# Optimization experiments

Hardware: AMD Instinct MI355X
Metric: run time of the kernel (lower is better)

## Reference

```python
import jax, jax.numpy as jnp
from jax import lax
import numpy as np

B, S, T = 64, 100, 96
SRC_V, PRIM_V, NPROD, NFLD = 32000, 16000, 201, 100
E, HE, H, F, ATT = 128, 128, 256, 64, 256
DIN = E + ATT + F + H  # 704 = action_emb + prev_att + field + parent_state


def setup_inputs():
    key = jax.random.key(0)
    ks = jax.random.split(key, 40)
    def p(k, shape):
        return (jax.random.normal(k, shape) * 0.05).astype(jnp.float32)
    sent_lens = jax.random.randint(ks[0], (B,), 1, S + 1)
    src_tokens = jax.random.randint(ks[1], (B, S), 0, SRC_V)
    prev_action_ids = jax.random.randint(ks[2], (B, T), 0, NPROD)
    frontier_ids = jax.random.randint(ks[3], (B, T), 0, NFLD)
    # parent_t[b, t] must point at an already-produced decoder state (< t)
    parent_t = jax.random.randint(ks[4], (B, T), 0, T) % jnp.maximum(jnp.arange(T), 1)
    atype = jax.random.randint(ks[5], (B, T), 0, 4)  # 0=apply,1=gen,2=copy,3=pad
    is_applyconstr = (atype == 0).astype(jnp.float32)
    is_gentoken = (atype == 1).astype(jnp.float32)
    is_copy = (atype == 2).astype(jnp.float32)
    is_copy_tok = (jax.random.uniform(ks[6], (B, T, S)) < 0.05).astype(jnp.float32) * is_copy[:, :, None]
    applyconstr_ids = jax.random.randint(ks[7], (B, T), 0, NPROD)
    gentok_ids = jax.random.randint(ks[8], (B, T), 0, PRIM_V)
    return dict(
        src_tokens=src_tokens, sent_lens=sent_lens, prev_action_ids=prev_action_ids,
        parent_t=parent_t, frontier_ids=frontier_ids, applyconstr_ids=applyconstr_ids,
        gentok_ids=gentok_ids, is_applyconstr=is_applyconstr, is_gentoken=is_gentoken,
        is_copy=is_copy, is_copy_tok=is_copy_tok,
        src_emb=p(ks[9], (SRC_V, E)), prod_emb=p(ks[10], (NPROD, E)),
        prim_emb=p(ks[11], (PRIM_V, E)), field_emb=p(ks[12], (NFLD, F)),
        Wih_f=p(ks[13], (4 * HE, E)), Whh_f=p(ks[14], (4 * HE, HE)), bih_f=p(ks[15], (4 * HE,)), bhh_f=p(ks[16], (4 * HE,)),
        Wih_b=p(ks[17], (4 * HE, E)), Whh_b=p(ks[18], (4 * HE, HE)), bih_b=p(ks[19], (4 * HE,)), bhh_b=p(ks[20], (4 * HE,)),
        Wih_d=p(ks[21], (4 * H, DIN)), Whh_d=p(ks[22], (4 * H, H)), bih_d=p(ks[23], (4 * H,)), bhh_d=p(ks[24], (4 * H,)),
        W_lin_attn=p(ks[25], (H, H)), W_att_vec=p(ks[26], (ATT, 2 * H)), W_ptr=p(ks[27], (ATT, H)),
        W_a2e=p(ks[28], (E, ATT)), W_gen=p(ks[29], (1, ATT)), b_gen=p(ks[30], (1,)),
    )


def _cell(x, h, c, Wih, Whh, bih, bhh):
    # torch.nn.LSTMCell gate order: i, f, g, o
    g = x @ Wih.T + bih + h @ Whh.T + bhh
    i, f, gg, o = jnp.split(g, 4, axis=-1)
    c = jax.nn.sigmoid(f) * c + jax.nn.sigmoid(i) * jnp.tanh(gg)
    return jax.nn.sigmoid(o) * jnp.tanh(c), c


def _forward(src_tokens, sent_lens, prev_action_ids, parent_t, frontier_ids,
             applyconstr_ids, gentok_ids, is_applyconstr, is_gentoken, is_copy, is_copy_tok,
             src_emb, prod_emb, prim_emb, field_emb,
             Wih_f, Whh_f, bih_f, bhh_f, Wih_b, Whh_b, bih_b, bhh_b,
             Wih_d, Whh_d, bih_d, bhh_d,
             W_lin_attn, W_att_vec, W_ptr, W_a2e, W_gen, b_gen):
    b, s = src_tokens.shape
    t_max = prev_action_ids.shape[1]
    emb = src_emb[src_tokens]                                  # [B,S,E]
    valid = jnp.arange(s)[None, :] < sent_lens[:, None]        # [B,S]

    def make_step(Wih, Whh, bih, bhh):
        def step(carry, xs):
            h, c = carry
            xt, vt = xs
            hn, cn = _cell(xt, h, c, Wih, Whh, bih, bhh)
            m = vt[:, None]
            hn = jnp.where(m, hn, h)
            cn = jnp.where(m, cn, c)
            return (hn, cn), hn
        return step

    z = jnp.zeros((b, HE), emb.dtype)
    (hf, cf), hs_f = lax.scan(make_step(Wih_f, Whh_f, bih_f, bhh_f), (z, z),
                              (emb.transpose(1, 0, 2), valid.T))
    (hb, cb), hs_b = lax.scan(make_step(Wih_b, Whh_b, bih_b, bhh_b), (z, z),
                              (emb[:, ::-1].transpose(1, 0, 2), valid[:, ::-1].T))
    hs_b = hs_b[::-1]                                          # re-align to forward order
    encodings = jnp.concatenate([hs_f, hs_b], -1).transpose(1, 0, 2) * valid[:, :, None]  # [B,S,H]
    h = jnp.concatenate([hf, hb], -1)                          # [B,H] final bi-state
    c = jnp.concatenate([cf, cb], -1)
    h_enc_final = h

    src_pad = ~valid
    enc_attn = encodings @ W_lin_attn.T                        # [B,S,H]

    def s_attention(hh):
        aw = jnp.einsum('bsh,bh->bs', enc_attn, hh)
        aw = jax.nn.softmax(jnp.where(src_pad, -jnp.inf, aw), axis=1)
        ctx = jnp.einsum('bs,bsh->bh', aw, encodings)
        return jnp.tanh(jnp.concatenate([ctx, hh], -1) @ W_att_vec.T)

    # decode step t = 0 with zero input
    h, c = _cell(jnp.zeros((b, DIN), emb.dtype), h, c, Wih_d, Whh_d, bih_d, bhh_d)
    buf = jnp.zeros((t_max, b, H), emb.dtype).at[0].set(h)     # states_sequence buffer
    s0 = s_attention(h)

    def dec_step(carry, xs):
        h, c, s_prev, buf = carry
        t, a_id, f_id, pt = xs
        parent = buf[pt, jnp.arange(b)]                        # data-dependent parent state
        inp = jnp.concatenate([prod_emb[a_id], s_prev, field_emb[f_id], parent], -1)
        h, c = _cell(inp, h, c, Wih_d, Whh_d, bih_d, bhh_d)
        buf = buf.at[t].set(h)
        s = s_attention(h)
        return (h, c, s, buf), s

    xs = (jnp.arange(1, t_max), prev_action_ids[:, 1:].T, frontier_ids[:, 1:].T, parent_t[:, 1:].T)
    _, s_rest = lax.scan(dec_step, (h, c, s0, buf), xs)
    s_att = jnp.concatenate([s0[None], s_rest], 0)             # [T,B,ATT]

    readout = s_att @ W_a2e.T                                  # [T,B,E]
    p_apply = jax.nn.softmax(jnp.einsum('tbe,ne->tbn', readout, prod_emb), axis=-1)
    p_tok = jax.nn.softmax(jnp.einsum('tbe,ve->tbv', readout, prim_emb), axis=-1)
    p_gen = jax.nn.sigmoid(s_att @ W_gen.T + b_gen)[..., 0]    # [T,B]
    hW = encodings @ W_ptr.T                                   # [B,S,ATT]
    sc = jnp.einsum('tbh,bsh->tbs', s_att, hW)
    p_copy_tok = jax.nn.softmax(jnp.where(src_pad[None], -jnp.inf, sc), axis=-1)

    tgt_copy = jnp.sum(p_copy_tok * is_copy_tok.transpose(1, 0, 2), axis=2)        # [T,B]
    tgt_apply = jnp.take_along_axis(p_apply, applyconstr_ids.T[:, :, None], axis=2)[..., 0]
    tgt_gen = jnp.take_along_axis(p_tok, gentok_ids.T[:, :, None], axis=2)[..., 0]

    ap = (tgt_apply * is_applyconstr.T
          + p_gen * tgt_gen * is_gentoken.T
          + (1.0 - p_gen) * tgt_copy * is_copy.T)
    pad = (is_applyconstr + is_gentoken + is_copy).T == 0
    ap = jnp.where(pad, 1e-7, ap)
    logp = jnp.log(ap) * (~pad)
    return jnp.sum(logp, axis=0), h_enc_final


def reference(src_tokens, sent_lens, prev_action_ids, parent_t, frontier_ids,
              applyconstr_ids, gentok_ids, is_applyconstr, is_gentoken, is_copy, is_copy_tok,
              src_emb, prod_emb, prim_emb, field_emb,
              Wih_f, Whh_f, bih_f, bhh_f, Wih_b, Whh_b, bih_b, bhh_b,
              Wih_d, Whh_d, bih_d, bhh_d,
              W_lin_attn, W_att_vec, W_ptr, W_a2e, W_gen, b_gen):
    return _forward(src_tokens, sent_lens, prev_action_ids, parent_t, frontier_ids,
                    applyconstr_ids, gentok_ids, is_applyconstr, is_gentoken, is_copy, is_copy_tok,
                    src_emb, prod_emb, prim_emb, field_emb,
                    Wih_f, Whh_f, bih_f, bhh_f, Wih_b, Whh_b, bih_b, bhh_b,
                    Wih_d, Whh_d, bih_d, bhh_d,
                    W_lin_attn, W_att_vec, W_ptr, W_a2e, W_gen, b_gen)
```

## Files before the change

kernel.cpp:

```cpp
#include <hip/hip_runtime.h>
#include <math.h>

typedef unsigned int uint;
typedef unsigned short ushort;
typedef unsigned char uchar;
typedef _Float16 v2h __attribute__((ext_vector_type(2)));
typedef short bf16x8 __attribute__((ext_vector_type(8)));
typedef float f32x4 __attribute__((ext_vector_type(4)));

__device__ __forceinline__ float sigf(float x) { return 1.f / (1.f + expf(-x)); }

__device__ __forceinline__ uint packh2(float a, float b) {
  v2h v; v[0] = (_Float16)a; v[1] = (_Float16)b;
  return __builtin_bit_cast(uint, v);
}
__device__ __forceinline__ ushort f2h(float x) {
  _Float16 h = (_Float16)x;
  return __builtin_bit_cast(ushort, h);
}
__device__ __forceinline__ float h2f(ushort u) {
  return (float)__builtin_bit_cast(_Float16, u);
}
__device__ __forceinline__ float dot2(uint w, uint x, float acc) {
  return __builtin_amdgcn_fdot2(__builtin_bit_cast(v2h, w), __builtin_bit_cast(v2h, x), acc, false);
}
__device__ __forceinline__ ushort f2bf(float f) {
  uint x = __builtin_bit_cast(uint, f);
  return (ushort)((x + 0x7fffu + ((x >> 16) & 1u)) >> 16);
}
__device__ __forceinline__ int dot8i4(uint w, uint x, int acc) {
#if __has_builtin(__builtin_amdgcn_sdot8)
  return __builtin_amdgcn_sdot8((int)w, (int)x, acc, false);
#else
#pragma unroll
  for (int j = 0; j < 8; j++) {
    int a = ((int)(w << (28 - 4 * j))) >> 28;
    int b = ((int)(x << (28 - 4 * j))) >> 28;
    acc += a * b;
  }
  return acc;
#endif
}
__device__ __forceinline__ char qi4b(float x) { return (char)(int)rintf(x * 7.f); }
__device__ __forceinline__ uint nib4(uint a) {
  a &= 0x0F0F0F0Fu;
  a |= a >> 4;
  a &= 0x00FF00FFu;
  a |= a >> 8;
  return a & 0xFFFFu;
}

__device__ __forceinline__ float wgval8(int k, int d, const float* Wih, const float* Whh) {
  if (k < 256) return Wih[d * 704 + 128 + k];
  if (k < 512) return Wih[d * 704 + 448 + (k - 256)];
  return Whh[d * 256 + (k - 512)];
}

__device__ __forceinline__ void tr_one(const float* __restrict__ src, float* __restrict__ dst,
                                       int i, int rows, int ld, int col0) {
  int r = i % rows, c = i / rows;
  dst[i] = src[r * ld + col0 + c];
}

__global__ __launch_bounds__(256) void k_prepack(
    const float* __restrict__ Wih_f, const float* __restrict__ Wih_b,
    const float* __restrict__ W_lin, const float* __restrict__ W_ptr,
    const float* __restrict__ W_att, const float* __restrict__ W_a2e,
    const float* __restrict__ Wih_d, const float* __restrict__ prim_emb,
    const float* __restrict__ bih_f, const float* __restrict__ bhh_f,
    const float* __restrict__ bih_b, const float* __restrict__ bhh_b,
    const float* __restrict__ bih_d, const float* __restrict__ bhh_d,
    float* __restrict__ WIHFT, float* __restrict__ WIHBT, float* __restrict__ WLINT,
    float* __restrict__ WPTRT, float* __restrict__ WATTCT, float* __restrict__ WA2ET,
    float* __restrict__ WPRODT, float* __restrict__ WFLDT,
    uint* __restrict__ WAH16, ushort* __restrict__ PRIM16,
    float* __restrict__ BFB, float* __restrict__ BBB, float* __restrict__ BDD,
    float* __restrict__ DEN) {
  int idx = blockIdx.x * 256 + threadIdx.x;
  if (idx < 65536) tr_one(Wih_f, WIHFT, idx, 512, 128, 0);
  else if (idx < 131072) tr_one(Wih_b, WIHBT, idx - 65536, 512, 128, 0);
  else if (idx < 196608) tr_one(W_lin, WLINT, idx - 131072, 256, 256, 0);
  else if (idx < 262144) tr_one(W_ptr, WPTRT, idx - 196608, 256, 256, 0);
  else if (idx < 327680) tr_one(W_att, WATTCT, idx - 262144, 256, 512, 0);
  else if (idx < 360448) tr_one(W_a2e, WA2ET, idx - 327680, 128, 256, 0);
  else if (idx < 491520) tr_one(Wih_d, WPRODT, idx - 360448, 1024, 704, 0);
  else if (idx < 557056) tr_one(Wih_d, WFLDT, idx - 491520, 1024, 704, 384);
  else if (idx < 589824) {
    int i2 = idx - 557056;
    int kk = i2 >> 8, r = i2 & 255;
    WAH16[i2] = packh2(W_att[r * 512 + 256 + 2 * kk], W_att[r * 512 + 257 + 2 * kk]);
  } else if (idx < 590848) {
    int i2 = idx - 589824;
    if (i2 < 512) { BFB[i2] = bih_f[i2] + bhh_f[i2]; BBB[i2] = bih_b[i2] + bhh_b[i2]; }
    BDD[i2] = bih_d[i2] + bhh_d[i2];
  } else if (idx < 596992) {
    DEN[idx - 590848] = 0.f;
  } else if (idx < 2644992) {
    int i2 = idx - 596992;
    PRIM16[i2] = f2bf(prim_emb[i2]);
  }
}

__global__ __launch_bounds__(256) void k_packgi4(
    const float* __restrict__ Wih, const float* __restrict__ Whh,
    uint* __restrict__ outp, float* __restrict__ wscale) {
  int d = blockIdx.x, tid = threadIdx.x;
  __shared__ float arr[768];
  __shared__ float red[256];
  float v0 = wgval8(tid, d, Wih, Whh);
  float v1 = wgval8(tid + 256, d, Wih, Whh);
  float v2 = wgval8(tid + 512, d, Wih, Whh);
  arr[tid] = v0; arr[tid + 256] = v1; arr[tid + 512] = v2;
  red[tid] = fmaxf(fabsf(v0), fmaxf(fabsf(v1), fabsf(v2)));
  __syncthreads();
  for (int off = 128; off; off >>= 1) {
    if (tid < off) red[tid] = fmaxf(red[tid], red[tid + off]);
    __syncthreads();
  }
  float wmax = red[0];
  float inv = (wmax > 0.f) ? (7.f / wmax) : 0.f;
  if (tid < 96) {
    uint u = 0;
#pragma unroll
    for (int b = 0; b < 8; b++) {
      int q = (int)rintf(arr[8 * tid + b] * inv);
      u |= ((uint)q & 0xFu) << (4 * b);
    }
    outp[((tid >> 2) * 1024 + d) * 4 + (tid & 3)] = u;
  }
  if (tid == 0) wscale[d] = wmax / 49.f;
}

__global__ __launch_bounds__(256) void k_pfw2(
    const float* __restrict__ prod_emb, const float* __restrict__ field_emb,
    const float* __restrict__ WPRODT, const float* __restrict__ WFLDT,
    float* __restrict__ PW, float* __restrict__ FW) {
  int bi = blockIdx.x, tid = threadIdx.x;
  const float* emb; const float* WT; float* outp; int K, a;
  if (bi < 201) { a = bi; emb = prod_emb; WT = WPRODT; outp = PW; K = 128; }
  else { a = bi - 201; emb = field_emb; WT = WFLDT; outp = FW; K = 64; }
  __shared__ float es[128];
  if (tid < K) es[tid] = emb[a * K + tid];
  __syncthreads();
  float acc[4] = {0, 0, 0, 0};
  for (int k = 0; k < K; k++) {
    float ev = es[k];
#pragma unroll
    for (int j = 0; j < 4; j++) acc[j] = fmaf(ev, WT[k * 1024 + tid + j * 256], acc[j]);
  }
#pragma unroll
  for (int j = 0; j < 4; j++) outp[a * 1024 + tid + j * 256] = acc[j];
}

__global__ __launch_bounds__(256) void k_xproj2(const int* __restrict__ toks,
    const float* __restrict__ embt,
    const float* __restrict__ WTF, const float* __restrict__ WTB,
    const float* __restrict__ biasF, const float* __restrict__ biasB,
    float* __restrict__ outF, float* __restrict__ outB) {
  int bi = blockIdx.x;
  const float* WT = (bi < 400) ? WTF : WTB;
  const float* bias = (bi < 400) ? biasF : biasB;
  float* outp = (bi < 400) ? outF : outB;
  int row0 = (bi % 400) * 16;
  __shared__ __align__(16) float a[16][128];
  __shared__ int tk[16];
  int tid = threadIdx.x;
  if (tid < 16) {
    int row = row0 + tid;
    int b = row & 63, s = row >> 6;
    tk[tid] = toks[b * 100 + s];
  }
  __syncthreads();
#pragma unroll
  for (int i = 0; i < 8; i++) {
    int idx = tid + i * 256;
    int r = idx >> 7, k = idx & 127;
    a[r][k] = embt[tk[r] * 128 + k];
  }
  __syncthreads();
  int c = tid;
  float acc0[16], acc1[16];
  float b0 = bias[c], b1 = bias[c + 256];
#pragma unroll
  for (int r = 0; r < 16; r++) { acc0[r] = b0; acc1[r] = b1; }
  for (int k = 0; k < 128; k++) {
    float w0 = WT[k * 512 + c];
    float w1 = WT[k * 512 + c + 256];
#pragma unroll
    for (int r = 0; r < 16; r++) {
      float av = a[r][k];
      acc0[r] = fmaf(av, w0, acc0[r]);
      acc1[r] = fmaf(av, w1, acc1[r]);
    }
  }
#pragma unroll
  for (int r = 0; r < 16; r++) {
    outp[(row0 + r) * 512 + c] = acc0[r];
    outp[(row0 + r) * 512 + c + 256] = acc1[r];
  }
}

__global__ __launch_bounds__(512) void k_enc_scan(
    const float* __restrict__ xpf, const float* __restrict__ xpb,
    const float* __restrict__ WhhF, const float* __restrict__ WhhB,
    const int* __restrict__ lens,
    float* __restrict__ enc, float* __restrict__ h0, float* __restrict__ c0,
    float* __restrict__ outp) {
  int b = blockIdx.x & 63, dir = blockIdx.x >> 6;
  const float* xp = dir ? xpb : xpf;
  const float* Whh = dir ? WhhB : WhhF;
  int t = threadIdx.x;
  float4 wv[32];
  {
    const float4* wr = (const float4*)(Whh + t * 128);
#pragma unroll
    for (int j = 0; j < 32; j++) wv[j] = wr[j];
  }
  __shared__ __align__(16) float hs[128];
  __shared__ float gs[512];
  float c = 0.f, hreg = 0.f;
  if (t < 128) hs[t] = 0.f;
  int len = lens[b];
  __syncthreads();
  for (int s = 0; s < 100; s++) {
    int pos = dir ? (99 - s) : s;
    float acc = xp[(pos * 64 + b) * 512 + t];
#pragma unroll
    for (int j = 0; j < 32; j++) {
      float4 h4 = *(const float4*)&hs[4 * j];
      acc = fmaf(wv[j].x, h4.x, acc);
      acc = fmaf(wv[j].y, h4.y, acc);
      acc = fmaf(wv[j].z, h4.z, acc);
      acc = fmaf(wv[j].w, h4.w, acc);
    }
    gs[t] = acc;
    __syncthreads();
    if (t < 128) {
      float ig = sigf(gs[t]);
      float fg = sigf(gs[128 + t]);
      float gg = tanhf(gs[256 + t]);
      float og = sigf(gs[384 + t]);
      float cn = fmaf(fg, c, ig * gg);
      float hn = og * tanhf(cn);
      if (pos < len) { c = cn; hreg = hn; }
      hs[t] = hreg;
      enc[(b * 100 + pos) * 256 + dir * 128 + t] = (pos < len) ? hreg : 0.f;
    }
    __syncthreads();
  }
  if (t < 128) {
    h0[b * 256 + dir * 128 + t] = hreg;
    c0[b * 256 + dir * 128 + t] = c;
    outp[64 + b * 256 + dir * 128 + t] = hreg;
  }
}

__global__ __launch_bounds__(256) void k_proj2(
    const float* __restrict__ enc, const float* __restrict__ WlinT,
    const float* __restrict__ WptrT, const float* __restrict__ WattCT,
    ushort* __restrict__ eat16, ushort* __restrict__ hw16, ushort* __restrict__ ew16) {
  int bx = blockIdx.x;
  int which = bx >> 8;
  int b = (bx >> 2) & 63;
  int j0 = (bx & 3) * 64;
  const float* WT = (which == 0) ? WlinT : (which == 1) ? WptrT : WattCT;
  __shared__ __align__(16) float el[20][256];
  int tid = threadIdx.x;
  int jj = tid & 63, sg = tid >> 6;
  for (int st = 0; st < 5; st++) {
    __syncthreads();
#pragma unroll
    for (int i = 0; i < 20; i++) {
      int idx = tid + i * 256;
      int r = idx >> 8, k = idx & 255;
      el[r][k] = enc[(b * 100 + st * 20 + r) * 256 + k];
    }
    __syncthreads();
    float acc[5] = {0, 0, 0, 0, 0};
    for (int k4 = 0; k4 < 64; k4++) {
      float w0 = WT[(4 * k4 + 0) * 256 + j0 + jj];
      float w1 = WT[(4 * k4 + 1) * 256 + j0 + jj];
      float w2 = WT[(4 * k4 + 2) * 256 + j0 + jj];
      float w3 = WT[(4 * k4 + 3) * 256 + j0 + jj];
#pragma unroll
      for (int q = 0; q < 5; q++) {
        float4 ev = *(const float4*)&el[sg * 5 + q][4 * k4];
        acc[q] = fmaf(ev.x, w0, fmaf(ev.y, w1, fmaf(ev.z, w2, fmaf(ev.w, w3, acc[q]))));
      }
    }
#pragma unroll
    for (int q = 0; q < 5; q++) {
      int s = st * 20 + sg * 5 + q;
      ushort hv = f2h(acc[q]);
      if (which == 0) eat16[(b * 100 + s) * 256 + j0 + jj] = hv;
      else if (which == 1) hw16[(b * 100 + s) * 256 + j0 + jj] = hv;
      else ew16[(b * 100 + s) * 256 + j0 + jj] = hv;
    }
  }
}

__global__ __launch_bounds__(1024, 4) void k_decoder(
    const uint* __restrict__ WG4, const float* __restrict__ wscale,
    const uint* __restrict__ WAH16,
    const float* __restrict__ bdd, const float* __restrict__ PW, const float* __restrict__ FW,
    const float* __restrict__ h0g, const float* __restrict__ c0g,
    const uint* __restrict__ EAT32, const uint* __restrict__ EW32,
    const int* __restrict__ aid, const int* __restrict__ ptp, const int* __restrict__ fid,
    const int* __restrict__ lens, float* __restrict__ sbuf) {
  __shared__ __align__(16) uint ea[100 * 136];
  __shared__ __align__(16) uint ewl[100 * 128];
  __shared__ __align__(16) uint xq[96];
  __shared__ __align__(16) char histq[96 * 256];
  __shared__ float gsm[1024];
  __shared__ float vp[4][256];
  __shared__ float aw[128];
  __shared__ __align__(16) uint hx32[128];
  __shared__ float csm[256];
  __shared__ __align__(16) char h0q[256];
  int e = blockIdx.x, tid = threadIdx.x;
  int len = lens[e];
  float bias0 = bdd[tid];
  float wsc = wscale[tid];
  for (int u = tid; u < 12800; u += 1024) {
    int s = u >> 7, kk = u & 127;
    ea[s * 136 + kk] = EAT32[(e * 100 + s) * 128 + kk];
    ewl[u] = EW32[e * 12800 + u];
  }
  if (tid < 256) {
    csm[tid] = c0g[e * 256 + tid];
    h0q[tid] = qi4b(h0g[e * 256 + tid]);
  }
  const uint4* wq = (const uint4*)WG4 + tid;
  uint4 wr[8];
#pragma unroll
  for (int qq = 0; qq < 8; qq++) wr[qq] = wq[qq * 1024];
  uint war[32];
  {
    int r_v = tid & 255, q_v = tid >> 8;
#pragma unroll
    for (int i = 0; i < 32; i++) war[i] = WAH16[(q_v * 32 + i) * 256 + r_v];
  }
  __syncthreads();
  if (tid < 96) {
    if (tid < 64) xq[tid] = 0u;
    else {
      const uint* p = (const uint*)&h0q[8 * (tid - 64)];
      xq[tid] = nib4(p[0]) | (nib4(p[1]) << 16);
    }
  }
  __syncthreads();
  int gacc;
  {
    int a0 = 0, a1 = 0, a2 = 0, a3 = 0;
#pragma unroll 4
    for (int qq = 8; qq < 24; qq++) {
      uint4 wv = wq[qq * 1024];
      uint4 xv = *(const uint4*)&xq[qq * 4];
      a0 = dot8i4(wv.x, xv.x, a0);
      a1 = dot8i4(wv.y, xv.y, a1);
      a2 = dot8i4(wv.z, xv.z, a2);
      a3 = dot8i4(wv.w, xv.w, a3);
    }
    gacc = a0 + a1 + a2 + a3;
  }
  float pf = 0.f;
  for (int t = 0; t < 96; t++) {
    int tn = (t < 95) ? (t + 1) : 95;
    int ptn = ptp[e * 96 + tn];
    {
      int a0 = gacc, a1 = 0, a2 = 0, a3 = 0;
#pragma unroll
      for (int qq = 0; qq < 8; qq++) {
        uint4 xv = *(const uint4*)&xq[qq * 4];
        a0 = dot8i4(wr[qq].x, xv.x, a0);
        a1 = dot8i4(wr[qq].y, xv.y, a1);
        a2 = dot8i4(wr[qq].z, xv.z, a2);
        a3 = dot8i4(wr[qq].w, xv.w, a3);
      }
      gsm[tid] = fmaf((float)(a0 + a1 + a2 + a3), wsc, bias0 + pf);
    }
    __syncthreads();
    if (tid < 256) {
      int d = tid;
      float gi = gsm[d], gf = gsm[256 + d], gg = gsm[512 + d], go = gsm[768 + d];
      float c = fmaf(sigf(gf), csm[d], sigf(gi) * tanhf(gg));
      csm[d] = c;
      float h = sigf(go) * tanhf(c);
      char q = qi4b(h);
      histq[t * 256 + d] = q;
      float hp = __shfl_xor(h, 1);
      if (!(d & 1)) hx32[d >> 1] = packh2(h, hp);
      uint v = ((uint)(uchar)q & 0xFu) << (4 * (d & 7));
      v |= (uint)__shfl_xor((int)v, 1);
      v |= (uint)__shfl_xor((int)v, 2);
      v |= (uint)__shfl_xor((int)v, 4);
      if (!(d & 7)) xq[64 + (d >> 3)] = v;
    }
    __syncthreads();
    if (tid < 800) {
      int s = tid >> 3, sub = tid & 7;
      if (s < len) {
        const uint4* ep = (const uint4*)&ea[s * 136 + sub * 16];
        const uint4* hp = (const uint4*)&hx32[sub * 16];
        float a = 0.f;
#pragma unroll
        for (int i = 0; i < 4; i++) {
          uint4 ev = ep[i], hv = hp[i];
          a = dot2(ev.x, hv.x, a);
          a = dot2(ev.y, hv.y, a);
          a = dot2(ev.z, hv.z, a);
          a = dot2(ev.w, hv.w, a);
        }
        a += __shfl_down(a, 4);
        a += __shfl_down(a, 2);
        a += __shfl_down(a, 1);
        if (sub == 0) aw[s] = a;
      }
    } else if (tid >= 960) {
      const uint* p = (const uint*)&histq[ptn * 256 + 8 * (tid - 960)];
      xq[32 + (tid - 960)] = nib4(p[0]) | (nib4(p[1]) << 16);
    }
    __syncthreads();
    {
      int a0 = 0, a1 = 0, a2 = 0, a3 = 0;
#pragma unroll 4
      for (int qq = 0; qq < 8; qq++) {
        uint4 wv = wq[(8 + qq) * 1024];
        uint4 xv = *(const uint4*)&xq[32 + qq * 4];
        a0 = dot8i4(wv.x, xv.x, a0);
        a1 = dot8i4(wv.y, xv.y, a1);
        a2 = dot8i4(wv.z, xv.z, a2);
        a3 = dot8i4(wv.w, xv.w, a3);
      }
      gacc = a0 + a1 + a2 + a3;
    }
    if (tid < 64) {
      float a0 = (tid < len) ? aw[tid] : -1e30f;
      float a1 = (64 + tid < len) ? aw[64 + tid] : -1e30f;
      float m = fmaxf(a0, a1);
#pragma unroll
      for (int off = 32; off; off >>= 1) m = fmaxf(m, __shfl_xor(m, off));
      float x0 = expf(a0 - m), x1 = expf(a1 - m);
      float ss = x0 + x1;
#pragma unroll
      for (int off = 32; off; off >>= 1) ss += __shfl_xor(ss, off);
      float rinv = 1.f / ss;
      aw[tid] = x0 * rinv;
      aw[64 + tid] = x1 * rinv;
    }
    __syncthreads();
    {
      int an = aid[e * 96 + tn], fn = fid[e * 96 + tn];
      float pw_n = PW[an * 1024 + tid];
      float fw_n = FW[fn * 1024 + tid];
      int r = tid & 255, q = tid >> 8;
      float part = 0.f;
      const ushort* ew = (const ushort*)ewl;
      for (int s = q * 25; s < q * 25 + 25; s++)
        part = fmaf(aw[s], h2f(ew[s * 256 + r]), part);
#pragma unroll
      for (int i = 0; i < 32; i++)
        part = dot2(war[i], hx32[q * 32 + i], part);
      vp[q][r] = part;
      {
        int a0 = 0, a1 = 0, a2 = 0, a3 = 0;
#pragma unroll 4
        for (int qq = 0; qq < 8; qq++) {
          uint4 wv = wq[(16 + qq) * 1024];
          uint4 xv = *(const uint4*)&xq[64 + qq * 4];
          a0 = dot8i4(wv.x, xv.x, a0);
          a1 = dot8i4(wv.y, xv.y, a1);
          a2 = dot8i4(wv.z, xv.z, a2);
          a3 = dot8i4(wv.w, xv.w, a3);
        }
        gacc += a0 + a1 + a2 + a3;
      }
      pf = pw_n + fw_n;
    }
    __syncthreads();
    if (tid < 256) {
      float s = tanhf(vp[0][tid] + vp[1][tid] + vp[2][tid] + vp[3][tid]);
      sbuf[(t * 64 + e) * 256 + tid] = s;
      uint v = ((uint)(uchar)qi4b(s) & 0xFu) << (4 * (tid & 7));
      v |= (uint)__shfl_xor((int)v, 1);
      v |= (uint)__shfl_xor((int)v, 2);
      v |= (uint)__shfl_xor((int)v, 4);
      if (!(tid & 7)) xq[tid >> 3] = v;
    }
    __syncthreads();
  }
}

__global__ __launch_bounds__(256) void k_readout(const float* __restrict__ sbuf,
    const float* __restrict__ wT, float* __restrict__ rd, ushort* __restrict__ rd16) {
  int row0 = blockIdx.x * 16;
  __shared__ __align__(16) float sl[16][256];
  int tid = threadIdx.x;
#pragma unroll
  for (int i = 0; i < 16; i++) {
    int idx = tid + i * 256;
    int r = idx >> 8, k = idx & 255;
    sl[r][k] = sbuf[(row0 + r) * 256 + k];
  }
  __syncthreads();
  int c = tid & 127, rg = tid >> 7;
  float acc[8] = {0, 0, 0, 0, 0, 0, 0, 0};
  for (int k4 = 0; k4 < 64; k4++) {
    float w0 = wT[(4 * k4 + 0) * 128 + c];
    float w1 = wT[(4 * k4 + 1) * 128 + c];
    float w2 = wT[(4 * k4 + 2) * 128 + c];
    float w3 = wT[(4 * k4 + 3) * 128 + c];
#pragma unroll
    for (int r = 0; r < 8; r++) {
      float4 s4 = *(const float4*)&sl[rg * 8 + r][4 * k4];
      acc[r] = fmaf(s4.x, w0, fmaf(s4.y, w1, fmaf(s4.z, w2, fmaf(s4.w, w3, acc[r]))));
    }
  }
#pragma unroll
  for (int r = 0; r < 8; r++) {
    int row = row0 + rg * 8 + r;
    rd[row * 128 + c] = acc[r];
    rd16[row * 128 + c] = f2bf(acc[r]);
  }
}

__global__ __launch_bounds__(256) void k_apply2(
    const float* __restrict__ rd, const float* __restrict__ prod,
    const int* __restrict__ ids, float* __restrict__ tga) {
  __shared__ __align__(16) float pl[201 * 128];
  __shared__ __align__(16) float rl[32][128];
  int tid = threadIdx.x;
  int row0 = blockIdx.x * 32;
  for (int u = tid; u < 201 * 128; u += 256) pl[u] = prod[u];
  for (int u = tid; u < 4096; u += 256) {
    int r = u >> 7, k = u & 127;
    rl[r][k] = rd[(row0 + r) * 128 + k];
  }
  __syncthreads();
  int wv = tid >> 6, l = tid & 63;
  float lg[8][4];
#pragma unroll
  for (int rr = 0; rr < 8; rr++)
#pragma unroll
    for (int s = 0; s < 4; s++) lg[rr][s] = 0.f;
  int nvalid = (l + 192 < 201) ? 4 : 3;
  for (int k4 = 0; k4 < 32; k4++) {
    float4 rv[8];
#pragma unroll
    for (int rr = 0; rr < 8; rr++) rv[rr] = *(const float4*)&rl[wv * 8 + rr][4 * k4];
#pragma unroll
    for (int s = 0; s < 4; s++) {
      if (s < nvalid) {
        float4 pv = *(const float4*)&pl[(l + 64 * s) * 128 + 4 * k4];
#pragma unroll
        for (int rr = 0; rr < 8; rr++)
          lg[rr][s] = fmaf(pv.x, rv[rr].x, fmaf(pv.y, rv[rr].y,
                      fmaf(pv.z, rv[rr].z, fmaf(pv.w, rv[rr].w, lg[rr][s]))));
      }
    }
  }
#pragma unroll
  for (int rr = 0; rr < 8; rr++) {
    float m = -1e30f;
#pragma unroll
    for (int s = 0; s < 4; s++) if (s < nvalid) m = fmaxf(m, lg[rr][s]);
#pragma unroll
    for (int off = 32; off; off >>= 1) m = fmaxf(m, __shfl_xor(m, off));
    float ss = 0.f;
#pragma unroll
    for (int s = 0; s < 4; s++) if (s < nvalid) ss += expf(lg[rr][s] - m);
#pragma unroll
    for (int off = 32; off; off >>= 1) ss += __shfl_xor(ss, off);
    int row = row0 + wv * 8 + rr;
    int tt = row >> 6, bb = row & 63;
    int id = ids[bb * 96 + tt];
    if (l == (id & 63)) {
      int s = id >> 6;
      tga[row] = expf(lg[rr][s] - m) / ss;
    }
  }
}

__global__ __launch_bounds__(256) void k_tok_den2(
    const ushort* __restrict__ rd16, const ushort* __restrict__ prim16,
    float* __restrict__ den) {
  int wave = threadIdx.x >> 6, lane = threadIdx.x & 63;
  int rowblk = blockIdx.x >> 3, strip = blockIdx.x & 7;
  int row0 = rowblk * 128 + wave * 32;
  int col0 = strip * 2000;
  int m = lane & 15, q = lane >> 4;
  bf16x8 a[2][4];
#pragma unroll
  for (int rg = 0; rg < 2; rg++)
#pragma unroll
    for (int i = 0; i < 4; i++)
      a[rg][i] = *(const bf16x8*)&rd16[(row0 + rg * 16 + m) * 128 + q * 8 + i * 32];
  float rs[2][4];
#pragma unroll
  for (int rg = 0; rg < 2; rg++)
#pragma unroll
    for (int r = 0; r < 4; r++) rs[rg][r] = 0.f;
  for (int ct = 0; ct < 125; ct++) {
    int cb = col0 + ct * 16 + m;
    f32x4 acc0 = {0.f, 0.f, 0.f, 0.f};
    f32x4 acc1 = {0.f, 0.f, 0.f, 0.f};
#pragma unroll
    for (int i = 0; i < 4; i++) {
      bf16x8 b = *(const bf16x8*)&prim16[cb * 128 + q * 8 + i * 32];
      acc0 = __builtin_amdgcn_mfma_f32_16x16x32_bf16(a[0][i], b, acc0, 0, 0, 0);
      acc1 = __builtin_amdgcn_mfma_f32_16x16x32_bf16(a[1][i], b, acc1, 0, 0, 0);
    }
#pragma unroll
    for (int r = 0; r < 4; r++) {
      rs[0][r] += expf(acc0[r]);
      rs[1][r] += expf(acc1[r]);
    }
  }
#pragma unroll
  for (int rg = 0; rg < 2; rg++)
#pragma unroll
    for (int r = 0; r < 4; r++) {
#pragma unroll
      for (int off = 1; off < 16; off <<= 1) rs[rg][r] += __shfl_xor(rs[rg][r], off);
    }
  if (m == 0) {
#pragma unroll
    for (int rg = 0; rg < 2; rg++)
#pragma unroll
      for (int r = 0; r < 4; r++)
        atomicAdd(&den[row0 + rg * 16 + q * 4 + r], rs[rg][r]);
  }
}

__global__ __launch_bounds__(256) void k_copy2f(
    const float* __restrict__ sbuf, const ushort* __restrict__ hw16,
    const float* __restrict__ ict, const int* __restrict__ lens,
    const float* __restrict__ rd, const float* __restrict__ prim,
    const float* __restrict__ wgen, const float* __restrict__ bgen,
    const int* __restrict__ gids, const float* __restrict__ den,
    const float* __restrict__ tga,
    const float* __restrict__ isap, const float* __restrict__ isgen,
    const float* __restrict__ iscp, float* __restrict__ outp) {
  __shared__ __align__(16) uint sx[96 * 128];
  __shared__ __align__(16) uint hw[100 * 132];
  __shared__ float sc[96 * 104];
  __shared__ __align__(16) uint wg16[128];
  __shared__ float tgcl[96];
  __shared__ float redf[256];
  int bb = blockIdx.x, tid = threadIdx.x;
  const uint* hwsrc = (const uint*)hw16;
  for (int u = tid; u < 12800; u += 256) {
    int s = u >> 7, kk = u & 127;
    hw[s * 132 + kk] = hwsrc[(bb * 100 + s) * 128 + kk];
  }
  for (int u = tid; u < 12288; u += 256) {
    int t = u >> 7, kk = u & 127;
    const float* p = &sbuf[(t * 64 + bb) * 256 + 2 * kk];
    sx[u] = packh2(p[0], p[1]);
  }
  if (tid < 128) wg16[tid] = packh2(wgen[2 * tid], wgen[2 * tid + 1]);
  __syncthreads();
  if (tid < 240) {
    int i = tid / 10, j = tid % 10;
    float acc[4][10] = {};
    for (int kk = 0; kk < 128; kk++) {
      uint hv[10], sv[4];
#pragma unroll
      for (int jj = 0; jj < 10; jj++) hv[jj] = hw[(j * 10 + jj) * 132 + kk];
#pragma unroll
      for (int ii = 0; ii < 4; ii++) sv[ii] = sx[(i * 4 + ii) * 128 + kk];
#pragma unroll
      for (int ii = 0; ii < 4; ii++)
#pragma unroll
        for (int jj = 0; jj < 10; jj++)
          acc[ii][jj] = dot2(sv[ii], hv[jj], acc[ii][jj]);
    }
#pragma unroll
    for (int ii = 0; ii < 4; ii++)
#pragma unroll
      for (int jj = 0; jj < 10; jj++)
        sc[(i * 4 + ii) * 104 + j * 10 + jj] = acc[ii][jj];
  }
  __syncthreads();
  int len = lens[bb];
  int wv = tid >> 6, l = tid & 63;
  for (int t = wv; t < 96; t += 4) {
    float a0 = (l < len) ? sc[t * 104 + l] : -1e30f;
    float a1 = -1e30f;
    if (l < 36 && 64 + l < len) a1 = sc[t * 104 + 64 + l];
    float m = fmaxf(a0, a1);
#pragma unroll
    for (int off = 32; off; off >>= 1) m = fmaxf(m, __shfl_xor(m, off));
    float x0 = expf(a0 - m), x1 = (l < 36) ? expf(a1 - m) : 0.f;
    float ss = x0 + x1;
#pragma unroll
    for (int off = 32; off; off >>= 1) ss += __shfl_xor(ss, off);
    float rinv = 1.f / ss;
    float w0 = x0 * rinv * ict[(bb * 96 + t) * 100 + l];
    float w1 = (l < 36) ? x1 * rinv * ict[(bb * 96 + t) * 100 + 64 + l] : 0.f;
    float tt = w0 + w1;
#pragma unroll
    for (int off = 32; off; off >>= 1) tt += __shfl_xor(tt, off);
    if (l == 0) tgcl[t] = tt;
  }
  __syncthreads();
  float lp = 0.f;
  if (tid < 96) {
    int t = tid, row = t * 64 + bb;
    float g = bgen[0];
    const uint* sxr = &sx[t * 128];
#pragma unroll 8
    for (int kk = 0; kk < 128; kk++) g = dot2(sxr[kk], wg16[kk], g);
    float pg = sigf(g);
    int gid = gids[bb * 96 + t];
    float l2 = 0.f;
    for (int k = 0; k < 128; k++) l2 = fmaf(rd[row * 128 + k], prim[gid * 128 + k], l2);
    float tgen = expf(l2) / den[row];
    float ia = isap[bb * 96 + t], ig = isgen[bb * 96 + t], ic = iscp[bb * 96 + t];
    float ap = tga[row] * ia + pg * tgen * ig + (1.f - pg) * tgcl[t] * ic;
    lp = (ia + ig + ic == 0.f) ? 0.f : logf(fmaxf(ap, 1e-30f));
  }
  redf[tid] = lp;
  __syncthreads();
#pragma unroll
  for (int off = 128; off > 0; off >>= 1) {
    if (tid < off) redf[tid] += redf[tid + off];
    __syncthreads();
  }
  if (tid == 0) outp[bb] = redf[0];
}

extern "C" void kernel_launch(void* const* d_in, const int* in_sizes, int n_in,
                              void* d_out, int out_size, void* d_ws, size_t ws_size,
                              hipStream_t stream) {
  const int* src_tokens = (const int*)d_in[0];
  const int* sent_lens = (const int*)d_in[1];
  const int* prev_action = (const int*)d_in[2];
  const int* parent_t = (const int*)d_in[3];
  const int* frontier = (const int*)d_in[4];
  const int* applyids = (const int*)d_in[5];
  const int* gentokids = (const int*)d_in[6];
  const float* is_ap = (const float*)d_in[7];
  const float* is_gen = (const float*)d_in[8];
  const float* is_cp = (const float*)d_in[9];
  const float* is_cp_tok = (const float*)d_in[10];
  const float* src_emb = (const float*)d_in[11];
  const float* prod_emb = (const float*)d_in[12];
  const float* prim_emb = (const float*)d_in[13];
  const float* field_emb = (const float*)d_in[14];
  const float* Wih_f = (const float*)d_in[15];
  const float* Whh_f = (const float*)d_in[16];
  const float* bih_f = (const float*)d_in[17];
  const float* bhh_f = (const float*)d_in[18];
  const float* Wih_b = (const float*)d_in[19];
  const float* Whh_b = (const float*)d_in[20];
  const float* bih_b = (const float*)d_in[21];
  const float* bhh_b = (const float*)d_in[22];
  const float* Wih_d = (const float*)d_in[23];
  const float* Whh_d = (const float*)d_in[24];
  const float* bih_d = (const float*)d_in[25];
  const float* bhh_d = (const float*)d_in[26];
  const float* W_lin = (const float*)d_in[27];
  const float* W_att = (const float*)d_in[28];
  const float* W_ptr = (const float*)d_in[29];
  const float* W_a2e = (const float*)d_in[30];
  const float* W_gen = (const float*)d_in[31];
  const float* b_gen = (const float*)d_in[32];
  float* out = (float*)d_out;
  float* w = (float*)d_ws;

  size_t o = 0;
  float* XPF = w + o; o += (size_t)100 * 64 * 512;
  float* XPB = w + o; o += (size_t)100 * 64 * 512;
  float* ENC = w + o; o += (size_t)64 * 100 * 256;
  float* H0 = w + o; o += 64 * 256;
  float* C0 = w + o; o += 64 * 256;
  float* WIHFT = w + o; o += 128 * 512;
  float* WIHBT = w + o; o += 128 * 512;
  float* WLINT = w + o; o += 256 * 256;
  float* WPTRT = w + o; o += 256 * 256;
  float* WATTCT = w + o; o += 256 * 256;
  float* WA2ET = w + o; o += 256 * 128;
  float* WPRODT = w + o; o += 128 * 1024;
  float* WFLDT = w + o; o += 64 * 1024;
  float* PW = w + o; o += (size_t)201 * 1024;
  float* FW = w + o; o += (size_t)100 * 1024;
  float* BFB = w + o; o += 512;
  float* BBB = w + o; o += 512;
  float* BDD = w + o; o += 1024;
  uint* WG4 = (uint*)(w + o); o += (size_t)24 * 4096;
  float* WSCALE = w + o; o += 1024;
  uint* WAH16 = (uint*)(w + o); o += 128 * 256;
  ushort* EAT16 = (ushort*)(w + o); o += (size_t)64 * 100 * 256 / 2;
  ushort* EW16 = (ushort*)(w + o); o += (size_t)64 * 100 * 256 / 2;
  ushort* HW16 = (ushort*)(w + o); o += (size_t)64 * 100 * 256 / 2;
  float* SBUF = w + o; o += (size_t)96 * 64 * 256;
  float* RDOUT = w + o; o += (size_t)96 * 64 * 128;
  ushort* RD16 = (ushort*)(w + o); o += (size_t)96 * 64 * 128 / 2 + 64;
  ushort* PRIM16 = (ushort*)(w + o); o += (size_t)16000 * 128 / 2 + 64;
  float* DEN = w + o; o += 6144;
  float* TGA = w + o; o += 6144;

  k_prepack<<<dim3(10332), dim3(256), 0, stream>>>(
      Wih_f, Wih_b, W_lin, W_ptr, W_att, W_a2e, Wih_d, prim_emb,
      bih_f, bhh_f, bih_b, bhh_b, bih_d, bhh_d,
      WIHFT, WIHBT, WLINT, WPTRT, WATTCT, WA2ET, WPRODT, WFLDT,
      WAH16, PRIM16, BFB, BBB, BDD, DEN);
  k_packgi4<<<dim3(1024), dim3(256), 0, stream>>>(Wih_d, Whh_d, WG4, WSCALE);

  k_pfw2<<<dim3(301), dim3(256), 0, stream>>>(prod_emb, field_emb, WPRODT, WFLDT, PW, FW);

  k_xproj2<<<dim3(800), dim3(256), 0, stream>>>(src_tokens, src_emb, WIHFT, WIHBT,
                                                BFB, BBB, XPF, XPB);

  k_enc_scan<<<dim3(128), dim3(512), 0, stream>>>(XPF, XPB, Whh_f, Whh_b, sent_lens, ENC, H0, C0, out);

  k_proj2<<<dim3(768), dim3(256), 0, stream>>>(ENC, WLINT, WPTRT, WATTCT, EAT16, HW16, EW16);

  k_decoder<<<dim3(64), dim3(1024), 0, stream>>>(WG4, WSCALE, WAH16, BDD, PW, FW, H0, C0,
                                                 (const uint*)EAT16, (const uint*)EW16,
                                                 prev_action, parent_t, frontier, sent_lens,
                                                 SBUF);

  k_readout<<<dim3(384), dim3(256), 0, stream>>>(SBUF, WA2ET, RDOUT, RD16);
  k_apply2<<<dim3(192), dim3(256), 0, stream>>>(RDOUT, prod_emb, applyids, TGA);
  k_tok_den2<<<dim3(384), dim3(256), 0, stream>>>(RD16, PRIM16, DEN);
  k_copy2f<<<dim3(64), dim3(256), 0, stream>>>(SBUF, HW16, is_cp_tok, sent_lens,
                                               RDOUT, prim_emb, W_gen, b_gen, gentokids,
                                               DEN, TGA, is_ap, is_gen, is_cp, out);
}
```

Baseline: 1.307 ms.

## Restructure decoder step to drop a barrier and store packed nibble history

The decoder loop now keeps the hidden-state history as packed 4-bit words, so the parent-state operand is read directly by index instead of being repacked by a dedicated thread group each step. The attention-score, W_ah·h, parent-gate and h-gate partial dot products are merged into one phase, removing one block-wide barrier per timestep. The parent weights are prefetched into registers. The context sum over encoder words moves after the softmax into the final 256-thread phase, which leaves 768 threads idle during that loop. This trades fewer barriers for a serial 100-element loop on a quarter of the block and more register pressure.

```diff
diff --git a/kernel.cpp b/kernel.cpp
--- a/kernel.cpp
+++ b/kernel.cpp
@@ -309,8 +309,8 @@
     const int* __restrict__ lens, float* __restrict__ sbuf) {
   __shared__ __align__(16) uint ea[100 * 136];
   __shared__ __align__(16) uint ewl[100 * 128];
-  __shared__ __align__(16) uint xq[96];
-  __shared__ __align__(16) char histq[96 * 256];
+  __shared__ __align__(16) uint xq[32];
+  __shared__ __align__(16) uint histn[96 * 32];
   __shared__ float gsm[1024];
   __shared__ float vp[4][256];
   __shared__ float aw[128];
@@ -341,21 +341,19 @@
     for (int i = 0; i < 32; i++) war[i] = WAH16[(q_v * 32 + i) * 256 + r_v];
   }
   __syncthreads();
-  if (tid < 96) {
-    if (tid < 64) xq[tid] = 0u;
-    else {
-      const uint* p = (const uint*)&h0q[8 * (tid - 64)];
-      xq[tid] = nib4(p[0]) | (nib4(p[1]) << 16);
-    }
+  if (tid < 32) {
+    xq[tid] = 0u;
+    const uint* p = (const uint*)&h0q[8 * tid];
+    histn[tid] = nib4(p[0]) | (nib4(p[1]) << 16);
   }
   __syncthreads();
   int gacc;
   {
     int a0 = 0, a1 = 0, a2 = 0, a3 = 0;
 #pragma unroll 4
-    for (int qq = 8; qq < 24; qq++) {
+    for (int qq = 16; qq < 24; qq++) {
       uint4 wv = wq[qq * 1024];
-      uint4 xv = *(const uint4*)&xq[qq * 4];
+      uint4 xv = *(const uint4*)&histn[(qq - 16) * 4];
       a0 = dot8i4(wv.x, xv.x, a0);
       a1 = dot8i4(wv.y, xv.y, a1);
       a2 = dot8i4(wv.z, xv.z, a2);
@@ -386,47 +384,60 @@
       float c = fmaf(sigf(gf), csm[d], sigf(gi) * tanhf(gg));
       csm[d] = c;
       float h = sigf(go) * tanhf(c);
-      char q = qi4b(h);
-      histq[t * 256 + d] = q;
       float hp = __shfl_xor(h, 1);
       if (!(d & 1)) hx32[d >> 1] = packh2(h, hp);
-      uint v = ((uint)(uchar)q & 0xFu) << (4 * (d & 7));
+      uint v = ((uint)(uchar)qi4b(h) & 0xFu) << (4 * (d & 7));
       v |= (uint)__shfl_xor((int)v, 1);
       v |= (uint)__shfl_xor((int)v, 2);
       v |= (uint)__shfl_xor((int)v, 4);
-      if (!(d & 7)) xq[64 + (d >> 3)] = v;
-    }
-    __syncthreads();
-    if (tid < 800) {
-      int s = tid >> 3, sub = tid & 7;
-      if (s < len) {
-        const uint4* ep = (const uint4*)&ea[s * 136 + sub * 16];
-        const uint4* hp = (const uint4*)&hx32[sub * 16];
-        float a = 0.f;
-#pragma unroll
-        for (int i = 0; i < 4; i++) {
-          uint4 ev = ep[i], hv = hp[i];
-          a = dot2(ev.x, hv.x, a);
-          a = dot2(ev.y, hv.y, a);
-          a = dot2(ev.z, hv.z, a);
-          a = dot2(ev.w, hv.w, a);
+      if (!(d & 7)) histn[t * 32 + (d >> 3)] = v;
+    }
+    __syncthreads();
+    {
+      uint4 wvp[8];
+#pragma unroll
+      for (int qq = 0; qq < 8; qq++) wvp[qq] = wq[(8 + qq) * 1024];
+      if (tid < 800) {
+        int s = tid >> 3, sub = tid & 7;
+        if (s < len) {
+          const uint4* ep = (const uint4*)&ea[s * 136 + sub * 16];
+          const uint4* hp = (const uint4*)&hx32[sub * 16];
+          float a = 0.f;
+#pragma unroll
+          for (int i = 0; i < 4; i++) {
+            uint4 ev = ep[i], hv = hp[i];
+            a = dot2(ev.x, hv.x, a);
+            a = dot2(ev.y, hv.y, a);
+            a = dot2(ev.z, hv.z, a);
+            a = dot2(ev.w, hv.w, a);
+          }
+          a += __shfl_down(a, 4);
+          a += __shfl_down(a, 2);
+          a += __shfl_down(a, 1);
+          if (sub == 0) aw[s] = a;
         }
-        a += __shfl_down(a, 4);
-        a += __shfl_down(a, 2);
-        a += __shfl_down(a, 1);
-        if (sub == 0) aw[s] = a;
       }
-    } else if (tid >= 960) {
-      const uint* p = (const uint*)&histq[ptn * 256 + 8 * (tid - 960)];
-      xq[32 + (tid - 960)] = nib4(p[0]) | (nib4(p[1]) << 16);
-    }
-    __syncthreads();
-    {
+      {
+        int r = tid & 255, q = tid >> 8;
+        float part = 0.f;
+#pragma unroll
+        for (int i = 0; i < 32; i++)
+          part = dot2(war[i], hx32[q * 32 + i], part);
+        vp[q][r] = part;
+      }
       int a0 = 0, a1 = 0, a2 = 0, a3 = 0;
+#pragma unroll
+      for (int qq = 0; qq < 8; qq++) {
+        uint4 xv = *(const uint4*)&histn[ptn * 32 + qq * 4];
+        a0 = dot8i4(wvp[qq].x, xv.x, a0);
+        a1 = dot8i4(wvp[qq].y, xv.y, a1);
+        a2 = dot8i4(wvp[qq].z, xv.z, a2);
+        a3 = dot8i4(wvp[qq].w, xv.w, a3);
+      }
 #pragma unroll 4
       for (int qq = 0; qq < 8; qq++) {
-        uint4 wv = wq[(8 + qq) * 1024];
-        uint4 xv = *(const uint4*)&xq[32 + qq * 4];
+        uint4 wv = wq[(16 + qq) * 1024];
+        uint4 xv = *(const uint4*)&histn[t * 32 + qq * 4];
         a0 = dot8i4(wv.x, xv.x, a0);
         a1 = dot8i4(wv.y, xv.y, a1);
         a2 = dot8i4(wv.z, xv.z, a2);
@@ -434,58 +445,45 @@
       }
       gacc = a0 + a1 + a2 + a3;
     }
-    if (tid < 64) {
-      float a0 = (tid < len) ? aw[tid] : -1e30f;
-      float a1 = (64 + tid < len) ? aw[64 + tid] : -1e30f;
-      float m = fmaxf(a0, a1);
-#pragma unroll
-      for (int off = 32; off; off >>= 1) m = fmaxf(m, __shfl_xor(m, off));
-      float x0 = expf(a0 - m), x1 = expf(a1 - m);
-      float ss = x0 + x1;
-#pragma unroll
-      for (int off = 32; off; off >>= 1) ss += __shfl_xor(ss, off);
-      float rinv = 1.f / ss;
-      aw[tid] = x0 * rinv;
-      aw[64 + tid] = x1 * rinv;
-    }
     __syncthreads();
     {
       int an = aid[e * 96 + tn], fn = fid[e * 96 + tn];
       float pw_n = PW[an * 1024 + tid];
       float fw_n = FW[fn * 1024 + tid];
-      int r = tid & 255, q = tid >> 8;
-      float part = 0.f;
-      const ushort* ew = (const ushort*)ewl;
-      for (int s = q * 25; s < q * 25 + 25; s++)
-        part = fmaf(aw[s], h2f(ew[s * 256 + r]), part);
-#pragma unroll
-      for (int i = 0; i < 32; i++)
-        part = dot2(war[i], hx32[q * 32 + i], part);
-      vp[q][r] = part;
-      {
-        int a0 = 0, a1 = 0, a2 = 0, a3 = 0;
-#pragma unroll 4
-        for (int qq = 0; qq < 8; qq++) {
-          uint4 wv = wq[(16 + qq) * 1024];
-          uint4 xv = *(const uint4*)&xq[64 + qq * 4];
-          a0 = dot8i4(wv.x, xv.x, a0);
-          a1 = dot8i4(wv.y, xv.y, a1);
-          a2 = dot8i4(wv.z, xv.z, a2);
-          a3 = dot8i4(wv.w, xv.w, a3);
-        }
-        gacc += a0 + a1 + a2 + a3;
+      if (tid < 64) {
+        float a0 = (tid < len) ? aw[tid] : -1e30f;
+        float a1 = (64 + tid < len) ? aw[64 + tid] : -1e30f;
+        float m = fmaxf(a0, a1);
+#pragma unroll
+        for (int off = 32; off; off >>= 1) m = fmaxf(m, __shfl_xor(m, off));
+        float x0 = expf(a0 - m), x1 = expf(a1 - m);
+        float ss = x0 + x1;
+#pragma unroll
+        for (int off = 32; off; off >>= 1) ss += __shfl_xor(ss, off);
+        float rinv = 1.f / ss;
+        aw[tid] = x0 * rinv;
+        aw[64 + tid] = x1 * rinv;
       }
       pf = pw_n + fw_n;
     }
     __syncthreads();
     if (tid < 256) {
-      float s = tanhf(vp[0][tid] + vp[1][tid] + vp[2][tid] + vp[3][tid]);
-      sbuf[(t * 64 + e) * 256 + tid] = s;
-      uint v = ((uint)(uchar)qi4b(s) & 0xFu) << (4 * (tid & 7));
+      int r = tid;
+      const ushort* ew = (const ushort*)ewl;
+      float c0 = 0.f, c1 = 0.f, c2 = 0.f, c3 = 0.f;
+      for (int s = 0; s < 25; s++) {
+        c0 = fmaf(aw[s], h2f(ew[s * 256 + r]), c0);
+        c1 = fmaf(aw[25 + s], h2f(ew[(25 + s) * 256 + r]), c1);
+        c2 = fmaf(aw[50 + s], h2f(ew[(50 + s) * 256 + r]), c2);
+        c3 = fmaf(aw[75 + s], h2f(ew[(75 + s) * 256 + r]), c3);
+      }
+      float sv = tanhf((vp[0][r] + c0) + (vp[1][r] + c1) + (vp[2][r] + c2) + (vp[3][r] + c3));
+      sbuf[(t * 64 + e) * 256 + r] = sv;
+      uint v = ((uint)(uchar)qi4b(sv) & 0xFu) << (4 * (r & 7));
       v |= (uint)__shfl_xor((int)v, 1);
       v |= (uint)__shfl_xor((int)v, 2);
       v |= (uint)__shfl_xor((int)v, 4);
-      if (!(tid & 7)) xq[tid >> 3] = v;
+      if (!(r & 7)) xq[r >> 3] = v;
     }
     __syncthreads();
   }
```

Result: slower. 1.403 ms (+7.3%).
